# Kernel optimization log

Hardware: AMD Instinct MI355X
Metric: run time of the kernel (lower is better)

Reference implementation:

```python
import jax, jax.numpy as jnp
import numpy as np
import math

D_MODEL = 2048
HEADS = 16
D_K = D_MODEL // HEADS  # 128
D_FF = 2048
N = 8192
EPS = 1e-6


def _norm(x, alpha, bias):
    # torch Norm: alpha * (x - mean) / (std + eps) + bias, std uses ddof=1
    mu = jnp.mean(x, axis=-1, keepdims=True)
    sd = jnp.std(x, axis=-1, ddof=1, keepdims=True)
    return alpha * (x - mu) / (sd + EPS) + bias


def setup_inputs() -> dict:
    key = jax.random.key(0)
    ks = jax.random.split(key, 16)
    s = 0.02
    inp = {
        "q": jax.random.normal(ks[0], (N, D_MODEL), jnp.float32),
        "k": jax.random.normal(ks[1], (N, D_MODEL), jnp.float32),
        "v": jax.random.normal(ks[2], (N, D_MODEL), jnp.float32),
        # norm params (norm_1 exists in module but is unused in forward)
        "nq_a": jnp.ones((D_MODEL,), jnp.float32), "nq_b": jnp.zeros((D_MODEL,), jnp.float32),
        "nk_a": jnp.ones((D_MODEL,), jnp.float32), "nk_b": jnp.zeros((D_MODEL,), jnp.float32),
        "nv_a": jnp.ones((D_MODEL,), jnp.float32), "nv_b": jnp.zeros((D_MODEL,), jnp.float32),
        "n2_a": jnp.ones((D_MODEL,), jnp.float32), "n2_b": jnp.zeros((D_MODEL,), jnp.float32),
        # attention projections, stored [in, out]
        "Wq": jax.random.normal(ks[3], (D_MODEL, D_MODEL), jnp.float32) * s,
        "bq": jnp.zeros((D_MODEL,), jnp.float32),
        "Wk": jax.random.normal(ks[4], (D_MODEL, D_MODEL), jnp.float32) * s,
        "bk": jnp.zeros((D_MODEL,), jnp.float32),
        "Wv": jax.random.normal(ks[5], (D_MODEL, D_MODEL), jnp.float32) * s,
        "bv": jnp.zeros((D_MODEL,), jnp.float32),
        "Wo": jax.random.normal(ks[6], (D_MODEL, D_MODEL), jnp.float32) * s,
        "bo": jnp.zeros((D_MODEL,), jnp.float32),
        # FFN
        "W1": jax.random.normal(ks[7], (D_MODEL, D_FF), jnp.float32) * s,
        "b1": jnp.zeros((D_FF,), jnp.float32),
        "W2": jax.random.normal(ks[8], (D_FF, D_MODEL), jnp.float32) * s,
        "b2": jnp.zeros((D_MODEL,), jnp.float32),
    }
    return inp


def reference(q, k, v,
              nq_a, nq_b, nk_a, nk_b, nv_a, nv_b, n2_a, n2_b,
              Wq, bq, Wk, bk, Wv, bv, Wo, bo, W1, b1, W2, b2):
    x = v  # residual stream (dropout is identity at inference)
    qn = _norm(q, nq_a, nq_b)
    kn = _norm(k, nk_a, nk_b)
    vn = _norm(v, nv_a, nv_b)

    # projections -> [N, h, d_k] then transpose(1,2) -> [N, d_k, h]
    qh = (qn @ Wq + bq).reshape(N, HEADS, D_K).transpose(0, 2, 1)
    kh = (kn @ Wk + bk).reshape(N, HEADS, D_K).transpose(0, 2, 1)
    vh = (vn @ Wv + bv).reshape(N, HEADS, D_K).transpose(0, 2, 1)

    # NON-STANDARD (as-written in source): per-token [d_k, d_k] attention
    # contracting over the head axis, scaled by 1/sqrt(d_k).
    scores = jnp.einsum('nah,nbh->nab', qh, kh) / math.sqrt(D_K)  # [N, d_k, d_k]
    probs = jax.nn.softmax(scores, axis=-1)
    attn = jnp.einsum('nab,nbh->nah', probs, vh)  # [N, d_k, h]

    concat = attn.transpose(0, 2, 1).reshape(N, D_MODEL)  # [N, h*d_k]
    x = x + (concat @ Wo + bo)

    x2 = _norm(x, n2_a, n2_b)
    ff = jax.nn.relu(x2 @ W1 + b1) @ W2 + b2
    return x + ff
```

## Files before the change

kernel.cpp:

```cpp
#include <hip/hip_runtime.h>
#include <hip/hip_bf16.h>

#define DM 2048
#define NTOK 8192
#define EPS 1e-6f

typedef __attribute__((ext_vector_type(8))) short short8;
typedef __attribute__((ext_vector_type(4))) short short4v;
typedef __attribute__((ext_vector_type(4))) float f32x4;
typedef __attribute__((ext_vector_type(16))) float f32x16;
typedef __attribute__((ext_vector_type(4))) unsigned int u32x4;

typedef const __attribute__((address_space(1))) void gvoid;
typedef __attribute__((address_space(3))) void lvoid;

static __device__ __forceinline__ unsigned short f2bf(float f) {
    unsigned u = __builtin_bit_cast(unsigned, f);
    unsigned r = u + 0x7FFFu + ((u >> 16) & 1u);
    return (unsigned short)(r >> 16);
}

__global__ __launch_bounds__(256) void norm_rows(
        const float* __restrict__ in, const float* __restrict__ alpha,
        const float* __restrict__ beta, unsigned short* __restrict__ out) {
    const int row = blockIdx.x;
    const int t = threadIdx.x;
    const float* x = in + (size_t)row * DM + t * 8;
    float4 v0 = *(const float4*)(x);
    float4 v1 = *(const float4*)(x + 4);
    float s = (v0.x + v0.y) + (v0.z + v0.w) + (v1.x + v1.y) + (v1.z + v1.w);
    float ss = v0.x*v0.x + v0.y*v0.y + v0.z*v0.z + v0.w*v0.w
             + v1.x*v1.x + v1.y*v1.y + v1.z*v1.z + v1.w*v1.w;
    #pragma unroll
    for (int m = 1; m < 64; m <<= 1) {
        s  += __shfl_xor(s, m);
        ss += __shfl_xor(ss, m);
    }
    __shared__ float red[8];
    const int wv = t >> 6, ln = t & 63;
    if (ln == 0) { red[wv] = s; red[4 + wv] = ss; }
    __syncthreads();
    s  = (red[0] + red[1]) + (red[2] + red[3]);
    ss = (red[4] + red[5]) + (red[6] + red[7]);
    const float mu = s * (1.0f / DM);
    float var = (ss - s * mu) * (1.0f / (DM - 1));
    var = fmaxf(var, 0.0f);
    const float scale = 1.0f / (sqrtf(var) + EPS);
    float4 a0 = *(const float4*)(alpha + t*8);
    float4 a1 = *(const float4*)(alpha + t*8 + 4);
    float4 b0 = *(const float4*)(beta + t*8);
    float4 b1 = *(const float4*)(beta + t*8 + 4);
    short8 o;
    o[0] = (short)f2bf(a0.x * (v0.x - mu) * scale + b0.x);
    o[1] = (short)f2bf(a0.y * (v0.y - mu) * scale + b0.y);
    o[2] = (short)f2bf(a0.z * (v0.z - mu) * scale + b0.z);
    o[3] = (short)f2bf(a0.w * (v0.w - mu) * scale + b0.w);
    o[4] = (short)f2bf(a1.x * (v1.x - mu) * scale + b1.x);
    o[5] = (short)f2bf(a1.y * (v1.y - mu) * scale + b1.y);
    o[6] = (short)f2bf(a1.z * (v1.z - mu) * scale + b1.z);
    o[7] = (short)f2bf(a1.w * (v1.w - mu) * scale + b1.w);
    *(short8*)(out + (size_t)row * DM + t * 8) = o;
}

__global__ __launch_bounds__(256) void wtrans(
        const float* __restrict__ W, unsigned short* __restrict__ Wt, int perm, float wscale) {
    __shared__ float tile[32][33];
    const int bc = blockIdx.x * 32, bk = blockIdx.y * 32;
    const int t = threadIdx.x;
    const int tc = t & 31, tr = t >> 5;
    #pragma unroll
    for (int i = 0; i < 4; ++i)
        tile[tr + i*8][tc] = W[(size_t)(bk + tr + i*8) * DM + bc + tc];
    __syncthreads();
    #pragma unroll
    for (int i = 0; i < 4; ++i) {
        const int c = bc + tr + i*8;
        const int pc = perm ? ((c & 127) * 16 + (c >> 7)) : c;
        Wt[(size_t)pc * DM + bk + tc] = f2bf(tile[tc][tr + i*8] * wscale);
    }
}

#define BARRIER __builtin_amdgcn_s_barrier()
#define WAIT_LGKM0 asm volatile("s_waitcnt lgkmcnt(0)" ::: "memory")
#define VMCNT(n) asm volatile("s_waitcnt vmcnt(" #n ")" ::: "memory")

template<int EPI>
__global__ __launch_bounds__(512, 2) void gemm256(
        const unsigned short* __restrict__ A, const unsigned short* __restrict__ Bt,
        const float* __restrict__ bias, const float* __restrict__ resid,
        float* __restrict__ outF, unsigned short* __restrict__ outB, int biasPerm,
        float bscale) {
    __shared__ __align__(16) char lds[131072];
    char* ldsA = lds;
    char* ldsB = lds + 65536;

    const int t = threadIdx.x, l = t & 63, w = t >> 6;
    const int wm = w >> 2, wn = w & 3;

    const int b = blockIdx.x;
    const int wg = (b & 7) * 32 + (b >> 3);
    const int n0 = (wg >> 5) * 256;
    const int m0 = (wg & 31) * 256;

    const int rS = t >> 3;
    const int cS = ((t & 7) ^ (rS & 7)) * 8;
    const unsigned short* aSt = A  + (size_t)(m0 + rS) * 2048 + cS;
    const unsigned short* bSt = Bt + (size_t)(n0 + rS) * 2048 + cS;
    const int ldsStW = w * 1024;

    const int aRd = wm * 16384 + (l & 15) * 128;
    const int bRd = (wn >> 1) * 16384 + (wn & 1) * 8192 + (l & 15) * 128;
    const int ch0 = (((l >> 4) + 0) ^ (l & 7)) * 16;
    const int ch1 = (((l >> 4) + 4) ^ (l & 7)) * 16;

    short8 af[4][2], bf[4][2];
    f32x4 acc[8][4] = {};

#define STG_A(buf, h, kt) do { \
    __builtin_amdgcn_global_load_lds((gvoid*)(aSt + (size_t)((h)*128)*2048 + (kt)*64), \
        (lvoid*)(ldsA + (buf)*32768 + (h)*16384 + ldsStW), 16, 0, 0); \
    __builtin_amdgcn_global_load_lds((gvoid*)(aSt + (size_t)((h)*128+64)*2048 + (kt)*64), \
        (lvoid*)(ldsA + (buf)*32768 + (h)*16384 + 8192 + ldsStW), 16, 0, 0); \
} while(0)
#define STG_B(buf, h, kt) do { \
    __builtin_amdgcn_global_load_lds((gvoid*)(bSt + (size_t)((h)*128)*2048 + (kt)*64), \
        (lvoid*)(ldsB + (buf)*32768 + (h)*16384 + ldsStW), 16, 0, 0); \
    __builtin_amdgcn_global_load_lds((gvoid*)(bSt + (size_t)((h)*128+64)*2048 + (kt)*64), \
        (lvoid*)(ldsB + (buf)*32768 + (h)*16384 + 8192 + ldsStW), 16, 0, 0); \
} while(0)
#define RD_A(buf, mh) do { \
    _Pragma("unroll") for (int ml = 0; ml < 4; ++ml) { \
        af[ml][0] = *(const short8*)(ldsA + (buf)*32768 + aRd + ((mh)*4+ml)*2048 + ch0); \
        af[ml][1] = *(const short8*)(ldsA + (buf)*32768 + aRd + ((mh)*4+ml)*2048 + ch1); \
    } } while(0)
#define RD_B(buf, nh) do { \
    _Pragma("unroll") for (int nl = 0; nl < 2; ++nl) { \
        bf[(nh)*2+nl][0] = *(const short8*)(ldsB + (buf)*32768 + bRd + ((nh)*2+nl)*2048 + ch0); \
        bf[(nh)*2+nl][1] = *(const short8*)(ldsB + (buf)*32768 + bRd + ((nh)*2+nl)*2048 + ch1); \
    } } while(0)
#define MM_Q(mh, nh) do { \
    __builtin_amdgcn_s_setprio(1); \
    _Pragma("unroll") for (int ml = 0; ml < 4; ++ml) \
    _Pragma("unroll") for (int nl = 0; nl < 2; ++nl) { \
        acc[(mh)*4+ml][(nh)*2+nl] = __builtin_amdgcn_mfma_f32_16x16x32_bf16( \
            af[ml][0], bf[(nh)*2+nl][0], acc[(mh)*4+ml][(nh)*2+nl], 0, 0, 0); \
        acc[(mh)*4+ml][(nh)*2+nl] = __builtin_amdgcn_mfma_f32_16x16x32_bf16( \
            af[ml][1], bf[(nh)*2+nl][1], acc[(mh)*4+ml][(nh)*2+nl], 0, 0, 0); \
    } \
    __builtin_amdgcn_s_setprio(0); \
} while(0)

    STG_B(0, 0, 0); STG_B(0, 1, 0); STG_A(0, 0, 0); STG_A(0, 1, 0);
    STG_B(1, 0, 1); STG_B(1, 1, 1);
    VMCNT(4);
    BARRIER;

    #pragma unroll 1
    for (int i = 0; i < 16; ++i) {
        const int kt1 = 2*i + 1, k2 = 2*i + 2, k3 = 2*i + 3;
        const bool more = (i < 15);
        RD_A(0, 0); RD_B(0, 0);
        STG_A(1, 0, kt1);
        BARRIER; WAIT_LGKM0;
        MM_Q(0, 0);
        BARRIER;
        RD_B(0, 1);
        STG_A(1, 1, kt1);
        BARRIER; WAIT_LGKM0;
        MM_Q(0, 1);
        BARRIER;
        RD_A(0, 1);
        if (more) STG_B(0, 0, k2);
        BARRIER; WAIT_LGKM0;
        MM_Q(1, 1);
        BARRIER;
        if (more) { STG_B(0, 1, k2); VMCNT(4); } else { VMCNT(0); }
        BARRIER;
        MM_Q(1, 0);
        BARRIER;
        RD_A(1, 0); RD_B(1, 0);
        if (more) STG_A(0, 0, k2);
        BARRIER; WAIT_LGKM0;
        MM_Q(0, 0);
        BARRIER;
        RD_B(1, 1);
        if (more) STG_A(0, 1, k2);
        BARRIER; WAIT_LGKM0;
        MM_Q(0, 1);
        BARRIER;
        RD_A(1, 1);
        if (more) STG_B(1, 0, k3);
        BARRIER; WAIT_LGKM0;
        MM_Q(1, 1);
        BARRIER;
        if (more) { STG_B(1, 1, k3); VMCNT(4); }
        BARRIER;
        MM_Q(1, 0);
        BARRIER;
    }

    #pragma unroll
    for (int ni = 0; ni < 4; ++ni) {
        const int col = n0 + wn*64 + ni*16 + (l & 15);
        const int cb = biasPerm ? ((col >> 4) + (col & 15) * 128) : col;
        const float bvv = bias[cb] * bscale;
        #pragma unroll
        for (int mi = 0; mi < 8; ++mi) {
            #pragma unroll
            for (int r = 0; r < 4; ++r) {
                const int rowg = m0 + wm*128 + mi*16 + (l >> 4)*4 + r;
                float vv = acc[mi][ni][r] + bvv;
                if (EPI == 1) vv = fmaxf(vv, 0.0f);
                const size_t idx = (size_t)rowg * 2048 + col;
                if (EPI == 2) outF[idx] = vv + resid[idx];
                else outB[idx] = f2bf(vv);
            }
        }
    }
#undef STG_A
#undef STG_B
#undef RD_A
#undef RD_B
#undef MM_Q
}

__global__ __launch_bounds__(256) void attn_tok(
        const unsigned short* __restrict__ Qt, const unsigned short* __restrict__ Kt,
        const unsigned short* __restrict__ Vp, unsigned short* __restrict__ Cc) {
    const int n = blockIdx.x;
    const int t = threadIdx.x, w = t >> 6, l = t & 63;
    const int q31 = l & 31, hi = l >> 5;
    __shared__ __align__(16) unsigned short c_s[16 * 132];

    const size_t tb = (size_t)n * DM;
    const short8 qf = *(const short8*)(Qt + tb + (w*32 + q31)*16 + hi*8);
    short8 kf[4];
    #pragma unroll
    for (int bt = 0; bt < 4; ++bt)
        kf[bt] = *(const short8*)(Kt + tb + (bt*32 + q31)*16 + hi*8);
    short8 vf[8];
    #pragma unroll
    for (int ks = 0; ks < 8; ++ks)
        vf[ks] = *(const short8*)(Vp + tb + (q31 & 15)*128 + ks*16 + hi*8);

    const f32x16 z = {};
    f32x16 sc[4];
    #pragma unroll
    for (int bt = 0; bt < 4; ++bt)
        sc[bt] = __builtin_amdgcn_mfma_f32_32x32x16_bf16(kf[bt], qf, z, 0, 0, 0);

    float m0 = sc[0][0], m1 = sc[1][0], m2 = sc[2][0], m3 = sc[3][0];
    #pragma unroll
    for (int r = 1; r < 16; ++r) {
        m0 = fmaxf(m0, sc[0][r]); m1 = fmaxf(m1, sc[1][r]);
        m2 = fmaxf(m2, sc[2][r]); m3 = fmaxf(m3, sc[3][r]);
    }
    float mx = fmaxf(fmaxf(m0, m1), fmaxf(m2, m3));
    { float a2 = mx, b2 = mx;
      asm volatile("v_permlane32_swap_b32 %0, %1" : "+v"(a2), "+v"(b2));
      mx = fmaxf(a2, b2); }

    float p[4][16];
    float s0 = 0.f, s1 = 0.f, s2 = 0.f, s3 = 0.f;
    #pragma unroll
    for (int r = 0; r < 16; ++r) {
        p[0][r] = __expf(sc[0][r] - mx); s0 += p[0][r];
        p[1][r] = __expf(sc[1][r] - mx); s1 += p[1][r];
        p[2][r] = __expf(sc[2][r] - mx); s2 += p[2][r];
        p[3][r] = __expf(sc[3][r] - mx); s3 += p[3][r];
    }
    float sm = (s0 + s1) + (s2 + s3);
    { float a2 = sm, b2 = sm;
      asm volatile("v_permlane32_swap_b32 %0, %1" : "+v"(a2), "+v"(b2));
      sm = a2 + b2; }
    const float inv = __builtin_amdgcn_rcpf(sm);
    #pragma unroll
    for (int bt = 0; bt < 4; ++bt)
        #pragma unroll
        for (int r = 0; r < 16; ++r)
            p[bt][r] *= inv;

    f32x16 acc = {};
    #pragma unroll
    for (int ks = 0; ks < 8; ++ks) {
        const int bt = ks >> 1, r0 = (ks & 1) * 8;
        unsigned X0, Y0, X1, Y1;
        asm("v_cvt_pk_bf16_f32 %0, %1, %2" : "=v"(X0) : "v"(p[bt][r0+0]), "v"(p[bt][r0+1]));
        asm("v_cvt_pk_bf16_f32 %0, %1, %2" : "=v"(Y0) : "v"(p[bt][r0+4]), "v"(p[bt][r0+5]));
        asm("v_cvt_pk_bf16_f32 %0, %1, %2" : "=v"(X1) : "v"(p[bt][r0+2]), "v"(p[bt][r0+3]));
        asm("v_cvt_pk_bf16_f32 %0, %1, %2" : "=v"(Y1) : "v"(p[bt][r0+6]), "v"(p[bt][r0+7]));
        asm volatile("v_permlane32_swap_b32 %0, %1" : "+v"(X0), "+v"(Y0));
        asm volatile("v_permlane32_swap_b32 %0, %1" : "+v"(X1), "+v"(Y1));
        u32x4 pw; pw[0] = X0; pw[1] = X1; pw[2] = Y0; pw[3] = Y1;
        const short8 paf = __builtin_bit_cast(short8, pw);
        acc = __builtin_amdgcn_mfma_f32_32x32x16_bf16(paf, vf[ks], acc, 0, 0, 0);
    }

    if (q31 < 16) {
        #pragma unroll
        for (int rp = 0; rp < 8; ++rp) {
            const int r = rp * 2;
            const int a = (r & 3) + 8 * (r >> 2) + 4 * hi;
            unsigned pk;
            asm("v_cvt_pk_bf16_f32 %0, %1, %2" : "=v"(pk) : "v"(acc[r]), "v"(acc[r+1]));
            *(unsigned*)((char*)c_s + q31*264 + (w*32 + a)*2) = pk;
        }
    }
    __syncthreads();
    *(short8*)(Cc + tb + t*8) = *(const short8*)((char*)c_s + (t >> 4)*264 + (t & 15)*16);
}

extern "C" void kernel_launch(void* const* d_in, const int* in_sizes, int n_in,
                              void* d_out, int out_size, void* d_ws, size_t ws_size,
                              hipStream_t stream) {
    (void)in_sizes; (void)n_in; (void)out_size; (void)ws_size;
    const float* q    = (const float*)d_in[0];
    const float* k    = (const float*)d_in[1];
    const float* v    = (const float*)d_in[2];
    const float* nq_a = (const float*)d_in[3];
    const float* nq_b = (const float*)d_in[4];
    const float* nk_a = (const float*)d_in[5];
    const float* nk_b = (const float*)d_in[6];
    const float* nv_a = (const float*)d_in[7];
    const float* nv_b = (const float*)d_in[8];
    const float* n2_a = (const float*)d_in[9];
    const float* n2_b = (const float*)d_in[10];
    const float* Wq   = (const float*)d_in[11];
    const float* bq   = (const float*)d_in[12];
    const float* Wk   = (const float*)d_in[13];
    const float* bk   = (const float*)d_in[14];
    const float* Wv   = (const float*)d_in[15];
    const float* bv   = (const float*)d_in[16];
    const float* Wo   = (const float*)d_in[17];
    const float* bo   = (const float*)d_in[18];
    const float* W1   = (const float*)d_in[19];
    const float* b1   = (const float*)d_in[20];
    const float* W2   = (const float*)d_in[21];
    const float* b2   = (const float*)d_in[22];

    char* ws = (char*)d_ws;
    const size_t MB = 1024 * 1024;
    unsigned short* buf0 = (unsigned short*)(ws);
    unsigned short* QtB  = (unsigned short*)(ws + 32*MB);
    unsigned short* KtB  = (unsigned short*)(ws + 64*MB);
    unsigned short* VpB  = (unsigned short*)(ws + 96*MB);
    unsigned short* Wqt  = (unsigned short*)(ws + 128*MB);
    unsigned short* Wkt  = (unsigned short*)(ws + 136*MB);
    unsigned short* Wvt  = (unsigned short*)(ws + 144*MB);
    unsigned short* Wot  = (unsigned short*)(ws + 152*MB);
    unsigned short* W1t  = (unsigned short*)(ws + 160*MB);
    unsigned short* W2t  = (unsigned short*)(ws + 168*MB);
    unsigned short* x2   = QtB;
    unsigned short* h1   = KtB;
    float* x = (float*)d_out;

    const float isq = 0.088388347648318447f;

    dim3 b256(256);
    dim3 gT(DM / 32, DM / 32);
    wtrans<<<gT, b256, 0, stream>>>(Wq, Wqt, 1, isq);
    wtrans<<<gT, b256, 0, stream>>>(Wk, Wkt, 1, 1.0f);
    wtrans<<<gT, b256, 0, stream>>>(Wv, Wvt, 0, 1.0f);
    wtrans<<<gT, b256, 0, stream>>>(Wo, Wot, 0, 1.0f);
    wtrans<<<gT, b256, 0, stream>>>(W1, W1t, 0, 1.0f);
    wtrans<<<gT, b256, 0, stream>>>(W2, W2t, 0, 1.0f);

    dim3 gN(NTOK);
    dim3 gG(256);
    dim3 b512(512);

    norm_rows<<<gN, b256, 0, stream>>>(q, nq_a, nq_b, buf0);
    gemm256<0><<<gG, b512, 0, stream>>>(buf0, Wqt, bq, nullptr, nullptr, QtB, 1, isq);
    norm_rows<<<gN, b256, 0, stream>>>(k, nk_a, nk_b, buf0);
    gemm256<0><<<gG, b512, 0, stream>>>(buf0, Wkt, bk, nullptr, nullptr, KtB, 1, 1.0f);
    norm_rows<<<gN, b256, 0, stream>>>(v, nv_a, nv_b, buf0);
    gemm256<0><<<gG, b512, 0, stream>>>(buf0, Wvt, bv, nullptr, nullptr, VpB, 0, 1.0f);
    attn_tok<<<gN, b256, 0, stream>>>(QtB, KtB, VpB, buf0);
    gemm256<2><<<gG, b512, 0, stream>>>(buf0, Wot, bo, v, x, nullptr, 0, 1.0f);
    norm_rows<<<gN, b256, 0, stream>>>(x, n2_a, n2_b, x2);
    gemm256<1><<<gG, b512, 0, stream>>>(x2, W1t, b1, nullptr, nullptr, h1, 0, 1.0f);
    gemm256<2><<<gG, b512, 0, stream>>>(h1, W2t, b2, x, x, nullptr, 0, 1.0f);
}
```

Baseline: 638.3 us.

## Store residual stream in bf16 and remap GEMM tiles per XCD

The intermediate residual x after the output projection is now kept in bf16 instead of fp32. A new bf16-input norm kernel reads it, and the final FFN GEMM reads this bf16 residual while writing fp32 output. This halves the traffic for the residual write and the reads in the norm and in the last GEMM epilogue, and it drops one fp32 read-modify-write of the output. The GEMM block-to-tile mapping also changes so that each XCD owns a contiguous group of M tiles, which is meant to improve L2 reuse of A. The cost is some precision on the residual, since it is rounded to bf16 before the final add.

```diff
diff --git a/kernel.cpp b/kernel.cpp
--- a/kernel.cpp
+++ b/kernel.cpp
@@ -18,6 +18,9 @@
     unsigned u = __builtin_bit_cast(unsigned, f);
     unsigned r = u + 0x7FFFu + ((u >> 16) & 1u);
     return (unsigned short)(r >> 16);
+}
+static __device__ __forceinline__ float bf2f(unsigned short h) {
+    return __builtin_bit_cast(float, (unsigned)h << 16);
 }
 
 __global__ __launch_bounds__(256) void norm_rows(
@@ -62,6 +65,42 @@
     *(short8*)(out + (size_t)row * DM + t * 8) = o;
 }
 
+__global__ __launch_bounds__(256) void norm_rows_bf16(
+        const unsigned short* __restrict__ in, const float* __restrict__ alpha,
+        const float* __restrict__ beta, unsigned short* __restrict__ out) {
+    const int row = blockIdx.x;
+    const int t = threadIdx.x;
+    short8 rv = *(const short8*)(in + (size_t)row * DM + t * 8);
+    float xv[8];
+    #pragma unroll
+    for (int j = 0; j < 8; ++j) xv[j] = bf2f((unsigned short)rv[j]);
+    float s = 0.f, ss = 0.f;
+    #pragma unroll
+    for (int j = 0; j < 8; ++j) { s += xv[j]; ss += xv[j]*xv[j]; }
+    #pragma unroll
+    for (int m = 1; m < 64; m <<= 1) {
+        s  += __shfl_xor(s, m);
+        ss += __shfl_xor(ss, m);
+    }
+    __shared__ float red[8];
+    const int wv = t >> 6, ln = t & 63;
+    if (ln == 0) { red[wv] = s; red[4 + wv] = ss; }
+    __syncthreads();
+    s  = (red[0] + red[1]) + (red[2] + red[3]);
+    ss = (red[4] + red[5]) + (red[6] + red[7]);
+    const float mu = s * (1.0f / DM);
+    float var = (ss - s * mu) * (1.0f / (DM - 1));
+    var = fmaxf(var, 0.0f);
+    const float scale = 1.0f / (sqrtf(var) + EPS);
+    short8 o;
+    #pragma unroll
+    for (int j = 0; j < 8; ++j) {
+        const float av = alpha[t*8 + j], bv = beta[t*8 + j];
+        o[j] = (short)f2bf(av * (xv[j] - mu) * scale + bv);
+    }
+    *(short8*)(out + (size_t)row * DM + t * 8) = o;
+}
+
 __global__ __launch_bounds__(256) void wtrans(
         const float* __restrict__ W, unsigned short* __restrict__ Wt, int perm, float wscale) {
     __shared__ float tile[32][33];
@@ -87,7 +126,8 @@
 template<int EPI>
 __global__ __launch_bounds__(512, 2) void gemm256(
         const unsigned short* __restrict__ A, const unsigned short* __restrict__ Bt,
-        const float* __restrict__ bias, const float* __restrict__ resid,
+        const float* __restrict__ bias, const float* __restrict__ residF,
+        const unsigned short* __restrict__ residB,
         float* __restrict__ outF, unsigned short* __restrict__ outB, int biasPerm,
         float bscale) {
     __shared__ __align__(16) char lds[131072];
@@ -98,9 +138,10 @@
     const int wm = w >> 2, wn = w & 3;
 
     const int b = blockIdx.x;
-    const int wg = (b & 7) * 32 + (b >> 3);
-    const int n0 = (wg >> 5) * 256;
-    const int m0 = (wg & 31) * 256;
+    const int xcd = b & 7;
+    const int j = b >> 3;
+    const int m0 = (xcd * 4 + (j & 3)) * 256;
+    const int n0 = (j >> 2) * 256;
 
     const int rS = t >> 3;
     const int cS = ((t & 7) ^ (rS & 7)) * 8;
@@ -212,8 +253,9 @@
                 float vv = acc[mi][ni][r] + bvv;
                 if (EPI == 1) vv = fmaxf(vv, 0.0f);
                 const size_t idx = (size_t)rowg * 2048 + col;
-                if (EPI == 2) outF[idx] = vv + resid[idx];
-                else outB[idx] = f2bf(vv);
+                if (EPI == 3)      outB[idx] = f2bf(vv + residF[idx]);
+                else if (EPI == 4) outF[idx] = vv + bf2f(residB[idx]);
+                else               outB[idx] = f2bf(vv);
             }
         }
     }
@@ -352,6 +394,7 @@
     unsigned short* W2t  = (unsigned short*)(ws + 168*MB);
     unsigned short* x2   = QtB;
     unsigned short* h1   = KtB;
+    unsigned short* xb   = VpB;
     float* x = (float*)d_out;
 
     const float isq = 0.088388347648318447f;
@@ -370,14 +413,14 @@
     dim3 b512(512);
 
     norm_rows<<<gN, b256, 0, stream>>>(q, nq_a, nq_b, buf0);
-    gemm256<0><<<gG, b512, 0, stream>>>(buf0, Wqt, bq, nullptr, nullptr, QtB, 1, isq);
+    gemm256<0><<<gG, b512, 0, stream>>>(buf0, Wqt, bq, nullptr, nullptr, nullptr, QtB, 1, isq);
     norm_rows<<<gN, b256, 0, stream>>>(k, nk_a, nk_b, buf0);
-    gemm256<0><<<gG, b512, 0, stream>>>(buf0, Wkt, bk, nullptr, nullptr, KtB, 1, 1.0f);
+    gemm256<0><<<gG, b512, 0, stream>>>(buf0, Wkt, bk, nullptr, nullptr, nullptr, KtB, 1, 1.0f);
     norm_rows<<<gN, b256, 0, stream>>>(v, nv_a, nv_b, buf0);
-    gemm256<0><<<gG, b512, 0, stream>>>(buf0, Wvt, bv, nullptr, nullptr, VpB, 0, 1.0f);
+    gemm256<0><<<gG, b512, 0, stream>>>(buf0, Wvt, bv, nullptr, nullptr, nullptr, VpB, 0, 1.0f);
     attn_tok<<<gN, b256, 0, stream>>>(QtB, KtB, VpB, buf0);
-    gemm256<2><<<gG, b512, 0, stream>>>(buf0, Wot, bo, v, x, nullptr, 0, 1.0f);
-    norm_rows<<<gN, b256, 0, stream>>>(x, n2_a, n2_b, x2);
-    gemm256<1><<<gG, b512, 0, stream>>>(x2, W1t, b1, nullptr, nullptr, h1, 0, 1.0f);
-    gemm256<2><<<gG, b512, 0, stream>>>(h1, W2t, b2, x, x, nullptr, 0, 1.0f);
-}
+    gemm256<3><<<gG, b512, 0, stream>>>(buf0, Wot, bo, v, nullptr, nullptr, xb, 0, 1.0f);
+    norm_rows_bf16<<<gN, b256, 0, stream>>>(xb, n2_a, n2_b, x2);
+    gemm256<1><<<gG, b512, 0, stream>>>(x2, W1t, b1, nullptr, nullptr, nullptr, h1, 0, 1.0f);
+    gemm256<4><<<gG, b512, 0, stream>>>(h1, W2t, b2, nullptr, xb, x, nullptr, 0, 1.0f);
+}
```

New measurement: 598.8 us. -6.2%, faster.
